# Kernel optimization log

Measured on AMD Instinct MI355X. Metric: run time of the kernel, lower is better.

The kernel has to match this reference:

```python
import jax, jax.numpy as jnp
import numpy as np

N_NODES = 100000
N_EDGES = 1600000
F_IN = 128
F_OUT = 64
BN_EPS = 1e-5


def setup_inputs() -> dict:
    key = jax.random.key(0)
    k1, k2, k3, k4, k5, k6 = jax.random.split(key, 6)
    x = jax.random.normal(k1, (N_NODES, F_IN), dtype=jnp.float32)
    edge_index = jax.random.randint(k2, (2, N_EDGES), 0, N_NODES, dtype=jnp.int64)
    edge_weight = jax.random.uniform(k3, (N_EDGES,), dtype=jnp.float32)
    # learned params: linear weight (no bias), batchnorm gamma/beta
    W = jax.random.normal(k4, (F_OUT, F_IN), dtype=jnp.float32) * (1.0 / np.sqrt(F_IN))
    gamma = jnp.ones((F_OUT,), dtype=jnp.float32)
    beta = jnp.zeros((F_OUT,), dtype=jnp.float32)
    return {"x": x, "edge_index": edge_index, "edge_weight": edge_weight,
            "W": W, "gamma": gamma, "beta": beta}


def reference(x, edge_index, edge_weight, W, gamma, beta):
    N = x.shape[0]
    h = x @ W.T  # [N, F_OUT]
    # add self loops with weight 1.0
    loop = jnp.arange(N, dtype=edge_index.dtype)
    src = jnp.concatenate([edge_index[0], loop])
    dst = jnp.concatenate([edge_index[1], loop])
    w = jnp.concatenate([edge_weight, jnp.ones((N,), dtype=h.dtype)])
    # degree of row (src) counts edge occurrences (unweighted)
    deg = jax.ops.segment_sum(jnp.ones_like(w), src, num_segments=N)
    dinv = jnp.where(deg > 0, jax.lax.rsqrt(deg), 0.0)
    norm = dinv[src] * w * dinv[dst]  # [E+N]
    # gather-scale-scatter aggregation
    out = jax.ops.segment_sum(h[src] * norm[:, None], dst, num_segments=N)
    out = jax.nn.relu(out)
    # BatchNorm1d (training mode: biased batch stats over nodes)
    mean = jnp.mean(out, axis=0)
    var = jnp.mean((out - mean) ** 2, axis=0)
    out = (out - mean) * jax.lax.rsqrt(var + BN_EPS) * gamma + beta
    # dropout p=0.0 -> identity
    return out
```

## Files before the change

kernel.cpp:

```cpp
#include <hip/hip_runtime.h>

#define N_NODES 100000
#define N_EDGES 1600000
#define F_IN 128
#define F_OUT 64
#define BN_EPS 1e-5f

#define NPART 2
#define NCHUNK 128
#define PSIZE 50000
#define CHUNK_E 12500

#define SCAN_NB 98


typedef __attribute__((ext_vector_type(8))) short bf16x8;
typedef __attribute__((ext_vector_type(4))) float f32x4;

__device__ __forceinline__ unsigned short f2bf(float x) {
    unsigned u = __float_as_uint(x);
    u += 0x7fffu + ((u >> 16) & 1u);
    return (unsigned short)(u >> 16);
}
__device__ __forceinline__ float bfl(unsigned short v) {
    return __int_as_float(((int)v) << 16);
}

__global__ __launch_bounds__(256) void convert_kernel(const void* __restrict__ ei,
                                                      int* __restrict__ s32,
                                                      int* __restrict__ d32) {
    const long long* q = (const long long*)ei;
    long long probe = q[threadIdx.x & 63];
    bool bad = (probe < 0 || probe >= N_NODES);
    int is64 = (__ballot(bad) == 0ULL);

    int i = blockIdx.x * 256 + threadIdx.x;
    if (i >= N_EDGES / 4) return;
    int4 s, d;
    if (is64) {
        longlong2 a = *(const longlong2*)&q[i * 4];
        longlong2 b = *(const longlong2*)&q[i * 4 + 2];
        s = make_int4((int)a.x, (int)a.y, (int)b.x, (int)b.y);
        longlong2 c = *(const longlong2*)&q[N_EDGES + i * 4];
        longlong2 e = *(const longlong2*)&q[N_EDGES + i * 4 + 2];
        d = make_int4((int)c.x, (int)c.y, (int)e.x, (int)e.y);
    } else {
        s = ((const int4*)ei)[i];
        d = ((const int4*)ei)[N_EDGES / 4 + i];
    }
    ((int4*)s32)[i] = s;
    ((int4*)d32)[i] = d;
}

__global__ __launch_bounds__(512) void count_kernel(const int* __restrict__ s32,
                                                    const int* __restrict__ d32,
                                                    unsigned* __restrict__ partial32,
                                                    unsigned char* __restrict__ rank) {
    __shared__ unsigned bins[PSIZE / 4];
    const int tid = threadIdx.x;
    const int p = blockIdx.x % NPART;
    const int b = blockIdx.x / NPART;
    const int p0 = p * PSIZE;
    for (int i = tid; i < PSIZE / 4; i += 512) bins[i] = 0u;
    __syncthreads();
    const int4* sp = (const int4*)(s32 + b * CHUNK_E);
    const int4* dp = (const int4*)(d32 + b * CHUNK_E);
    const int e0 = b * CHUNK_E;
    for (int i = tid; i < CHUNK_E / 4; i += 512) {
        int4 s = sp[i];
        int4 d = dp[i];
        int e = e0 + i * 4;
#define C1(sk, dk, kk) { \
        unsigned si = (unsigned)((sk) - p0); \
        if (si < PSIZE) atomicAdd(&bins[si >> 2], 1u << ((si & 3) * 8)); \
        unsigned dd = (unsigned)((dk) - p0); \
        if ((unsigned)(sk) < N_NODES && dd < PSIZE) { \
            unsigned sh = (dd & 3) * 8 + 4; \
            unsigned old = atomicAdd(&bins[dd >> 2], 16u << ((dd & 3) * 8)); \
            rank[e + kk] = (unsigned char)((old >> sh) & 0xFu); } }
        C1(s.x, d.x, 0) C1(s.y, d.y, 1) C1(s.z, d.z, 2) C1(s.w, d.w, 3)
#undef C1
    }
    __syncthreads();
    unsigned* dst = partial32 + (unsigned)blockIdx.x * (PSIZE / 4);
    for (int i = tid; i < PSIZE / 4; i += 512) dst[i] = bins[i];
}

__global__ __launch_bounds__(256) void redscan_kernel(unsigned* __restrict__ partial32,
                                                      float* __restrict__ dinv,
                                                      unsigned* __restrict__ off,
                                                      unsigned* __restrict__ bsum,
                                                      float* __restrict__ sums) {
    __shared__ unsigned s[256];
    const int tid = threadIdx.x;
    if (blockIdx.x == 0 && tid < 128) sums[tid] = 0.f;
    const int n0 = blockIdx.x * 1024 + tid * 4;
    unsigned cntk[4] = {0, 0, 0, 0};
    unsigned degk[4] = {0, 0, 0, 0};
    if (n0 < N_NODES) {
        unsigned idx = (unsigned)n0 >> 2;
#pragma unroll 8
        for (int c = 0; c < NCHUNK; ++c) {
            unsigned v = partial32[idx];
            unsigned nv = 0;
#pragma unroll
            for (int k = 0; k < 4; ++k) {
                unsigned byte = (v >> (k * 8)) & 0xFFu;
                nv |= (cntk[k] & 0xFFu) << (k * 8);
                cntk[k] += byte >> 4;
                degk[k] += byte & 0xFu;
            }
            partial32[idx] = nv;
            idx += (NPART * PSIZE) / 4;
        }
#pragma unroll
        for (int k = 0; k < 4; ++k)
            dinv[n0 + k] = rsqrtf((float)(degk[k] + 1u));
    }
    unsigned tsum = cntk[0] + cntk[1] + cntk[2] + cntk[3];
    s[tid] = tsum;
    __syncthreads();
    for (int d = 1; d < 256; d <<= 1) {
        unsigned t = (tid >= d) ? s[tid - d] : 0u;
        __syncthreads();
        s[tid] += t;
        __syncthreads();
    }
    unsigned run = s[tid] - tsum;
    if (n0 < N_NODES) {
        uint4 o;
        o.x = run;
        o.y = run + cntk[0];
        o.z = o.y + cntk[1];
        o.w = o.z + cntk[2];
        *(uint4*)&off[n0] = o;
    }
    if (tid == 255) bsum[blockIdx.x] = s[255];
}

__global__ __launch_bounds__(128) void scan2_kernel(unsigned* __restrict__ bsum) {
    __shared__ unsigned s[128];
    const int tid = threadIdx.x;
    unsigned v = (tid < SCAN_NB) ? bsum[tid] : 0u;
    s[tid] = v;
    __syncthreads();
    for (int d = 1; d < 128; d <<= 1) {
        unsigned t = (tid >= d) ? s[tid - d] : 0u;
        __syncthreads();
        s[tid] += t;
        __syncthreads();
    }
    if (tid < SCAN_NB) bsum[tid] = s[tid] - v;
}

__global__ __launch_bounds__(256) void place_kernel(const int* __restrict__ s32,
                                                    const int* __restrict__ d32,
                                                    const float* __restrict__ ew,
                                                    const unsigned* __restrict__ off,
                                                    const unsigned* __restrict__ bsum,
                                                    const unsigned* __restrict__ partial32,
                                                    const unsigned char* __restrict__ rank,
                                                    int2* __restrict__ buck) {
    int i = blockIdx.x * 256 + threadIdx.x;
    if (i >= N_EDGES / 4) return;
    int4 s = ((const int4*)s32)[i];
    int4 d = ((const int4*)d32)[i];
    float4 w = ((const float4*)ew)[i];
    uchar4 r = ((const uchar4*)rank)[i];
    const unsigned char* pb = (const unsigned char*)partial32;
    int e = i * 4;
    int b = e / CHUNK_E;
    unsigned base = (unsigned)b * NPART * PSIZE;
#define P1(sk, dk, wk, rk) { \
    if ((unsigned)(sk) < N_NODES && (unsigned)(dk) < N_NODES) { \
        unsigned pref = pb[base + (unsigned)(dk)]; \
        unsigned slot = off[dk] + bsum[(unsigned)(dk) >> 10] + pref + (rk); \
        if (slot < N_EDGES) \
            buck[slot] = make_int2((sk), __float_as_int(wk)); } }
    P1(s.x, d.x, w.x, r.x) P1(s.y, d.y, w.y, r.y)
    P1(s.z, d.z, w.z, r.z) P1(s.w, d.w, w.w, r.w)
#undef P1
}

__global__ __launch_bounds__(256) void gemm_kernel(const float* __restrict__ x,
                                                   const float* __restrict__ W,
                                                   const float* __restrict__ dinv,
                                                   unsigned short* __restrict__ hb) {
    __shared__ short wlds[16 * 64 * 8];
    const int tid = threadIdx.x;
    const int n0 = blockIdx.x * 64;
    {
        int out = tid & 63;
        int kb = tid >> 6;
#pragma unroll
        for (int i = 0; i < 4; ++i) {
            int koct = kb + i * 4;
            const float* wp = &W[out * F_IN + koct * 8];
            float4 aa = *(const float4*)wp;
            float4 bb = *(const float4*)(wp + 4);
            bf16x8 f;
            f[0] = (short)f2bf(aa.x); f[1] = (short)f2bf(aa.y);
            f[2] = (short)f2bf(aa.z); f[3] = (short)f2bf(aa.w);
            f[4] = (short)f2bf(bb.x); f[5] = (short)f2bf(bb.y);
            f[6] = (short)f2bf(bb.z); f[7] = (short)f2bf(bb.w);
            ((bf16x8*)wlds)[koct * 64 + out] = f;
        }
    }
    __syncthreads();
    const int wv = tid >> 6;
    const int lane = tid & 63;
    const int m = lane & 15;
    const int quad = lane >> 4;
    const int row = n0 + wv * 16 + m;
    const bool rv = row < N_NODES;
    const float* xrow = &x[(long)row * F_IN + quad * 8];
    f32x4 acc0 = {0.f, 0.f, 0.f, 0.f};
    f32x4 acc1 = {0.f, 0.f, 0.f, 0.f};
    f32x4 acc2 = {0.f, 0.f, 0.f, 0.f};
    f32x4 acc3 = {0.f, 0.f, 0.f, 0.f};
#pragma unroll
    for (int kc = 0; kc < 4; ++kc) {
        bf16x8 a = {0, 0, 0, 0, 0, 0, 0, 0};
        if (rv) {
            float4 aa = *(const float4*)(xrow + kc * 32);
            float4 bb = *(const float4*)(xrow + kc * 32 + 4);
            a[0] = (short)f2bf(aa.x); a[1] = (short)f2bf(aa.y);
            a[2] = (short)f2bf(aa.z); a[3] = (short)f2bf(aa.w);
            a[4] = (short)f2bf(bb.x); a[5] = (short)f2bf(bb.y);
            a[6] = (short)f2bf(bb.z); a[7] = (short)f2bf(bb.w);
        }
        const bf16x8* wrow = &((const bf16x8*)wlds)[(kc * 4 + quad) * 64 + m];
        acc0 = __builtin_amdgcn_mfma_f32_16x16x32_bf16(a, wrow[0],  acc0, 0, 0, 0);
        acc1 = __builtin_amdgcn_mfma_f32_16x16x32_bf16(a, wrow[16], acc1, 0, 0, 0);
        acc2 = __builtin_amdgcn_mfma_f32_16x16x32_bf16(a, wrow[32], acc2, 0, 0, 0);
        acc3 = __builtin_amdgcn_mfma_f32_16x16x32_bf16(a, wrow[48], acc3, 0, 0, 0);
    }
#pragma unroll
    for (int r = 0; r < 4; ++r) {
        int node = n0 + wv * 16 + quad * 4 + r;
        if (node < N_NODES) {
            float dv = dinv[node];
            unsigned short* hr = &hb[(long)node * F_OUT + m];
            hr[0]  = f2bf(acc0[r] * dv);
            hr[16] = f2bf(acc1[r] * dv);
            hr[32] = f2bf(acc2[r] * dv);
            hr[48] = f2bf(acc3[r] * dv);
        }
    }
}

#define AGG_BLOCKS 2048
#define NPW 13
__global__ __launch_bounds__(256) void aggregate_kernel(
    const unsigned short* __restrict__ hb, const float* __restrict__ dinv,
    const unsigned* __restrict__ off, const unsigned* __restrict__ bsum,
    const int2* __restrict__ buck, float* __restrict__ out,
    float* __restrict__ sums) {
    const int tid = threadIdx.x;
    const int wv = tid >> 6;
    const int lane = tid & 63;
    const int es = lane >> 3;
    const int cl = lane & 7;
    float s1[8] = {0.f, 0.f, 0.f, 0.f, 0.f, 0.f, 0.f, 0.f};
    float s2[8] = {0.f, 0.f, 0.f, 0.f, 0.f, 0.f, 0.f, 0.f};

    const int wid = blockIdx.x * 4 + wv;
    const int nbeg = wid * NPW;
    const int nend = (nbeg + NPW < N_NODES) ? nbeg + NPW : N_NODES;
    for (int n = nbeg; n < nend; ++n) {
        const unsigned o = off[n] + bsum[(unsigned)n >> 10];
        const unsigned onext = (n + 1 < N_NODES)
            ? off[n + 1] + bsum[(unsigned)(n + 1) >> 10]
            : (unsigned)N_EDGES;
        const unsigned c = onext - o;
        float a0[8] = {0.f, 0.f, 0.f, 0.f, 0.f, 0.f, 0.f, 0.f};
        float a1[8] = {0.f, 0.f, 0.f, 0.f, 0.f, 0.f, 0.f, 0.f};
        unsigned j = es;
        for (; j + 8 < c; j += 16) {
            int2 b1 = buck[o + j];
            int2 b2 = buck[o + j + 8];
            uint4 p1 = *(const uint4*)(hb + ((long)b1.x << 6) + cl * 8);
            uint4 p2 = *(const uint4*)(hb + ((long)b2.x << 6) + cl * 8);
            float w1 = __int_as_float(b1.y);
            float w2 = __int_as_float(b2.y);
            a0[0] += bfl((unsigned short)p1.x) * w1;
            a0[1] += bfl((unsigned short)(p1.x >> 16)) * w1;
            a0[2] += bfl((unsigned short)p1.y) * w1;
            a0[3] += bfl((unsigned short)(p1.y >> 16)) * w1;
            a0[4] += bfl((unsigned short)p1.z) * w1;
            a0[5] += bfl((unsigned short)(p1.z >> 16)) * w1;
            a0[6] += bfl((unsigned short)p1.w) * w1;
            a0[7] += bfl((unsigned short)(p1.w >> 16)) * w1;
            a1[0] += bfl((unsigned short)p2.x) * w2;
            a1[1] += bfl((unsigned short)(p2.x >> 16)) * w2;
            a1[2] += bfl((unsigned short)p2.y) * w2;
            a1[3] += bfl((unsigned short)(p2.y >> 16)) * w2;
            a1[4] += bfl((unsigned short)p2.z) * w2;
            a1[5] += bfl((unsigned short)(p2.z >> 16)) * w2;
            a1[6] += bfl((unsigned short)p2.w) * w2;
            a1[7] += bfl((unsigned short)(p2.w >> 16)) * w2;
        }
        if (j < c) {
            int2 b1 = buck[o + j];
            uint4 p1 = *(const uint4*)(hb + ((long)b1.x << 6) + cl * 8);
            float w1 = __int_as_float(b1.y);
            a0[0] += bfl((unsigned short)p1.x) * w1;
            a0[1] += bfl((unsigned short)(p1.x >> 16)) * w1;
            a0[2] += bfl((unsigned short)p1.y) * w1;
            a0[3] += bfl((unsigned short)(p1.y >> 16)) * w1;
            a0[4] += bfl((unsigned short)p1.z) * w1;
            a0[5] += bfl((unsigned short)(p1.z >> 16)) * w1;
            a0[6] += bfl((unsigned short)p1.w) * w1;
            a0[7] += bfl((unsigned short)(p1.w >> 16)) * w1;
        }
#pragma unroll
        for (int k = 0; k < 8; ++k) {
            a0[k] += a1[k];
            a0[k] += __shfl_xor(a0[k], 8);
            a0[k] += __shfl_xor(a0[k], 16);
            a0[k] += __shfl_xor(a0[k], 32);
        }
        if (es == 0) {
            float dn = dinv[n];
            uint4 pn = *(const uint4*)(hb + ((long)n << 6) + cl * 8);
            float hn[8] = {bfl((unsigned short)pn.x), bfl((unsigned short)(pn.x >> 16)),
                           bfl((unsigned short)pn.y), bfl((unsigned short)(pn.y >> 16)),
                           bfl((unsigned short)pn.z), bfl((unsigned short)(pn.z >> 16)),
                           bfl((unsigned short)pn.w), bfl((unsigned short)(pn.w >> 16))};
            float4 o0, o1;
            float* op = &o0.x;
#pragma unroll
            for (int k = 0; k < 8; ++k) {
                float v = fmaxf(dn * (a0[k] + hn[k]), 0.f);
                ((k < 4) ? (&o0.x) : (&o1.x))[k & 3] = v;
                s1[k] += v;
                s2[k] += v * v;
            }
            (void)op;
            float* orow = &out[(long)n * F_OUT + cl * 8];
            *(float4*)orow = o0;
            *(float4*)(orow + 4) = o1;
        }
    }
    __shared__ float l1[256];
    __shared__ float l2[256];
    if (es == 0) {
#pragma unroll
        for (int k = 0; k < 8; ++k) {
            l1[wv * 64 + cl * 8 + k] = s1[k];
            l2[wv * 64 + cl * 8 + k] = s2[k];
        }
    }
    __syncthreads();
    if (tid < 64) {
        float b1 = l1[tid] + l1[64 + tid] + l1[128 + tid] + l1[192 + tid];
        float b2 = l2[tid] + l2[64 + tid] + l2[128 + tid] + l2[192 + tid];
        atomicAdd(&sums[tid], b1);
        atomicAdd(&sums[64 + tid], b2);
    }
}

__global__ __launch_bounds__(256) void apply_kernel(float* __restrict__ agg,
                                                    const float* __restrict__ sums,
                                                    const float* __restrict__ gamma,
                                                    const float* __restrict__ beta) {
    __shared__ float sc[64], bi[64];
    if (threadIdx.x < 64) {
        int c = threadIdx.x;
        const float inv_n = 1.0f / (float)N_NODES;
        float mean = sums[c] * inv_n;
        float var = sums[64 + c] * inv_n - mean * mean;
        float rs = rsqrtf(var + BN_EPS);
        float scale = rs * gamma[c];
        sc[c] = scale;
        bi[c] = beta[c] - mean * scale;
    }
    __syncthreads();
    int i = blockIdx.x * blockDim.x + threadIdx.x;
    if (i >= N_NODES * 16) return;
    int c4 = (i & 15) << 2;
    float4 v = ((float4*)agg)[i];
    v.x = v.x * sc[c4 + 0] + bi[c4 + 0];
    v.y = v.y * sc[c4 + 1] + bi[c4 + 1];
    v.z = v.z * sc[c4 + 2] + bi[c4 + 2];
    v.w = v.w * sc[c4 + 3] + bi[c4 + 3];
    ((float4*)agg)[i] = v;
}

extern "C" void kernel_launch(void* const* d_in, const int* in_sizes, int n_in,
                              void* d_out, int out_size, void* d_ws, size_t ws_size,
                              hipStream_t stream) {
    const float* x     = (const float*)d_in[0];
    const void*  ei    = d_in[1];
    const float* ew    = (const float*)d_in[2];
    const float* W     = (const float*)d_in[3];
    const float* gamma = (const float*)d_in[4];
    const float* beta  = (const float*)d_in[5];
    float* out = (float*)d_out;
    float* ws  = (float*)d_ws;

    int*            s32       = (int*)ws;
    int*            d32       = (int*)(ws + 1600000);
    unsigned*       partial32 = (unsigned*)(ws + 3200000);
    unsigned short* hb        = (unsigned short*)(ws + 3200000);
    int2*           buck      = (int2*)(ws + 6400000);
    float*          dinv      = ws + 9600000;
    float*          sums      = ws + 9700000;
    unsigned*       off       = (unsigned*)(ws + 9800128);
    unsigned*       bsum      = (unsigned*)(ws + 9900128);
    unsigned char*  rank      = (unsigned char*)d_out;

    convert_kernel<<<(N_EDGES / 4 + 255) / 256, 256, 0, stream>>>(ei, s32, d32);
    count_kernel<<<NPART * NCHUNK, 512, 0, stream>>>(s32, d32, partial32, rank);
    redscan_kernel<<<SCAN_NB, 256, 0, stream>>>(partial32, dinv, off, bsum, sums);
    scan2_kernel<<<1, 128, 0, stream>>>(bsum);
    place_kernel<<<(N_EDGES / 4 + 255) / 256, 256, 0, stream>>>(s32, d32, ew, off, bsum,
                                                                partial32, rank, buck);
    gemm_kernel<<<(N_NODES + 63) / 64, 256, 0, stream>>>(x, W, dinv, hb);
    aggregate_kernel<<<AGG_BLOCKS, 256, 0, stream>>>(hb, dinv, off, bsum, buck, out, sums);
    apply_kernel<<<(N_NODES * 16 + 255) / 256, 256, 0, stream>>>(out, sums, gamma, beta);
}
```

Baseline: 304.8 us.

## Fuse index conversion into count kernel and remap aggregate lanes

```diff
diff --git a/kernel.cpp b/kernel.cpp
--- a/kernel.cpp
+++ b/kernel.cpp
@@ -22,54 +22,45 @@
     u += 0x7fffu + ((u >> 16) & 1u);
     return (unsigned short)(u >> 16);
 }
-__device__ __forceinline__ float bfl(unsigned short v) {
-    return __int_as_float(((int)v) << 16);
-}
-
-__global__ __launch_bounds__(256) void convert_kernel(const void* __restrict__ ei,
-                                                      int* __restrict__ s32,
-                                                      int* __restrict__ d32) {
+__device__ __forceinline__ float4 bf4(uint2 p) {
+    return make_float4(__int_as_float((int)(p.x << 16)),
+                       __int_as_float((int)(p.x & 0xffff0000u)),
+                       __int_as_float((int)(p.y << 16)),
+                       __int_as_float((int)(p.y & 0xffff0000u)));
+}
+
+__global__ __launch_bounds__(512) void count_kernel(const void* __restrict__ ei,
+                                                    int* __restrict__ s32,
+                                                    int* __restrict__ d32,
+                                                    unsigned* __restrict__ partial32) {
+    __shared__ unsigned bins[PSIZE / 4];
     const long long* q = (const long long*)ei;
     long long probe = q[threadIdx.x & 63];
-    bool bad = (probe < 0 || probe >= N_NODES);
-    int is64 = (__ballot(bad) == 0ULL);
-
-    int i = blockIdx.x * 256 + threadIdx.x;
-    if (i >= N_EDGES / 4) return;
-    int4 s, d;
-    if (is64) {
-        longlong2 a = *(const longlong2*)&q[i * 4];
-        longlong2 b = *(const longlong2*)&q[i * 4 + 2];
-        s = make_int4((int)a.x, (int)a.y, (int)b.x, (int)b.y);
-        longlong2 c = *(const longlong2*)&q[N_EDGES + i * 4];
-        longlong2 e = *(const longlong2*)&q[N_EDGES + i * 4 + 2];
-        d = make_int4((int)c.x, (int)c.y, (int)e.x, (int)e.y);
-    } else {
-        s = ((const int4*)ei)[i];
-        d = ((const int4*)ei)[N_EDGES / 4 + i];
-    }
-    ((int4*)s32)[i] = s;
-    ((int4*)d32)[i] = d;
-}
-
-__global__ __launch_bounds__(512) void count_kernel(const int* __restrict__ s32,
-                                                    const int* __restrict__ d32,
-                                                    unsigned* __restrict__ partial32,
-                                                    unsigned char* __restrict__ rank) {
-    __shared__ unsigned bins[PSIZE / 4];
+    bool badp = (probe < 0 || probe >= N_NODES);
+    int is64 = (__ballot(badp) == 0ULL);
+
     const int tid = threadIdx.x;
     const int p = blockIdx.x % NPART;
     const int b = blockIdx.x / NPART;
     const int p0 = p * PSIZE;
     for (int i = tid; i < PSIZE / 4; i += 512) bins[i] = 0u;
     __syncthreads();
-    const int4* sp = (const int4*)(s32 + b * CHUNK_E);
-    const int4* dp = (const int4*)(d32 + b * CHUNK_E);
     const int e0 = b * CHUNK_E;
     for (int i = tid; i < CHUNK_E / 4; i += 512) {
-        int4 s = sp[i];
-        int4 d = dp[i];
         int e = e0 + i * 4;
+        int4 s, d;
+        if (is64) {
+            longlong2 a = *(const longlong2*)&q[e];
+            longlong2 bb = *(const longlong2*)&q[e + 2];
+            s = make_int4((int)a.x, (int)a.y, (int)bb.x, (int)bb.y);
+            longlong2 c2 = *(const longlong2*)&q[N_EDGES + e];
+            longlong2 e2 = *(const longlong2*)&q[N_EDGES + e + 2];
+            d = make_int4((int)c2.x, (int)c2.y, (int)e2.x, (int)e2.y);
+        } else {
+            s = ((const int4*)ei)[e >> 2];
+            d = ((const int4*)ei)[(N_EDGES >> 2) + (e >> 2)];
+        }
+        if (p == 0) ((int4*)s32)[e >> 2] = s;
 #define C1(sk, dk, kk) { \
         unsigned si = (unsigned)((sk) - p0); \
         if (si < PSIZE) atomicAdd(&bins[si >> 2], 1u << ((si & 3) * 8)); \
@@ -77,7 +68,7 @@
         if ((unsigned)(sk) < N_NODES && dd < PSIZE) { \
             unsigned sh = (dd & 3) * 8 + 4; \
             unsigned old = atomicAdd(&bins[dd >> 2], 16u << ((dd & 3) * 8)); \
-            rank[e + kk] = (unsigned char)((old >> sh) & 0xFu); } }
+            d32[e + kk] = (dk) | (int)(((old >> sh) & 0xFu) << 27); } }
         C1(s.x, d.x, 0) C1(s.y, d.y, 1) C1(s.z, d.z, 2) C1(s.w, d.w, 3)
 #undef C1
     }
@@ -159,26 +150,25 @@
                                                     const unsigned* __restrict__ off,
                                                     const unsigned* __restrict__ bsum,
                                                     const unsigned* __restrict__ partial32,
-                                                    const unsigned char* __restrict__ rank,
                                                     int2* __restrict__ buck) {
     int i = blockIdx.x * 256 + threadIdx.x;
     if (i >= N_EDGES / 4) return;
     int4 s = ((const int4*)s32)[i];
     int4 d = ((const int4*)d32)[i];
     float4 w = ((const float4*)ew)[i];
-    uchar4 r = ((const uchar4*)rank)[i];
     const unsigned char* pb = (const unsigned char*)partial32;
     int e = i * 4;
     int b = e / CHUNK_E;
     unsigned base = (unsigned)b * NPART * PSIZE;
-#define P1(sk, dk, wk, rk) { \
-    if ((unsigned)(sk) < N_NODES && (unsigned)(dk) < N_NODES) { \
-        unsigned pref = pb[base + (unsigned)(dk)]; \
-        unsigned slot = off[dk] + bsum[(unsigned)(dk) >> 10] + pref + (rk); \
+#define P1(sk, dvk, wk) { \
+    unsigned dd = (unsigned)(dvk) & 0x07FFFFFFu; \
+    unsigned rk = ((unsigned)(dvk)) >> 27; \
+    if ((unsigned)(sk) < N_NODES && dd < N_NODES) { \
+        unsigned pref = pb[base + dd]; \
+        unsigned slot = off[dd] + bsum[dd >> 10] + pref + rk; \
         if (slot < N_EDGES) \
             buck[slot] = make_int2((sk), __float_as_int(wk)); } }
-    P1(s.x, d.x, w.x, r.x) P1(s.y, d.y, w.y, r.y)
-    P1(s.z, d.z, w.z, r.z) P1(s.w, d.w, w.w, r.w)
+    P1(s.x, d.x, w.x) P1(s.y, d.y, w.y) P1(s.z, d.z, w.z) P1(s.w, d.w, w.w)
 #undef P1
 }
 
@@ -259,10 +249,10 @@
     const int tid = threadIdx.x;
     const int wv = tid >> 6;
     const int lane = tid & 63;
-    const int es = lane >> 3;
-    const int cl = lane & 7;
-    float s1[8] = {0.f, 0.f, 0.f, 0.f, 0.f, 0.f, 0.f, 0.f};
-    float s2[8] = {0.f, 0.f, 0.f, 0.f, 0.f, 0.f, 0.f, 0.f};
+    const int es = lane >> 4;
+    const int cl = lane & 15;
+    float s1[4] = {0.f, 0.f, 0.f, 0.f};
+    float s2[4] = {0.f, 0.f, 0.f, 0.f};
 
     const int wid = blockIdx.x * 4 + wv;
     const int nbeg = wid * NPW;
@@ -273,82 +263,50 @@
             ? off[n + 1] + bsum[(unsigned)(n + 1) >> 10]
             : (unsigned)N_EDGES;
         const unsigned c = onext - o;
-        float a0[8] = {0.f, 0.f, 0.f, 0.f, 0.f, 0.f, 0.f, 0.f};
-        float a1[8] = {0.f, 0.f, 0.f, 0.f, 0.f, 0.f, 0.f, 0.f};
+        float4 a0 = make_float4(0.f, 0.f, 0.f, 0.f);
+        float4 a1 = make_float4(0.f, 0.f, 0.f, 0.f);
         unsigned j = es;
-        for (; j + 8 < c; j += 16) {
+        for (; j + 4 < c; j += 8) {
             int2 b1 = buck[o + j];
-            int2 b2 = buck[o + j + 8];
-            uint4 p1 = *(const uint4*)(hb + ((long)b1.x << 6) + cl * 8);
-            uint4 p2 = *(const uint4*)(hb + ((long)b2.x << 6) + cl * 8);
+            int2 b2 = buck[o + j + 4];
+            float4 h1 = bf4(((const uint2*)(hb + ((long)b1.x << 6)))[cl]);
+            float4 h2 = bf4(((const uint2*)(hb + ((long)b2.x << 6)))[cl]);
             float w1 = __int_as_float(b1.y);
             float w2 = __int_as_float(b2.y);
-            a0[0] += bfl((unsigned short)p1.x) * w1;
-            a0[1] += bfl((unsigned short)(p1.x >> 16)) * w1;
-            a0[2] += bfl((unsigned short)p1.y) * w1;
-            a0[3] += bfl((unsigned short)(p1.y >> 16)) * w1;
-            a0[4] += bfl((unsigned short)p1.z) * w1;
-            a0[5] += bfl((unsigned short)(p1.z >> 16)) * w1;
-            a0[6] += bfl((unsigned short)p1.w) * w1;
-            a0[7] += bfl((unsigned short)(p1.w >> 16)) * w1;
-            a1[0] += bfl((unsigned short)p2.x) * w2;
-            a1[1] += bfl((unsigned short)(p2.x >> 16)) * w2;
-            a1[2] += bfl((unsigned short)p2.y) * w2;
-            a1[3] += bfl((unsigned short)(p2.y >> 16)) * w2;
-            a1[4] += bfl((unsigned short)p2.z) * w2;
-            a1[5] += bfl((unsigned short)(p2.z >> 16)) * w2;
-            a1[6] += bfl((unsigned short)p2.w) * w2;
-            a1[7] += bfl((unsigned short)(p2.w >> 16)) * w2;
+            a0.x += h1.x * w1; a0.y += h1.y * w1; a0.z += h1.z * w1; a0.w += h1.w * w1;
+            a1.x += h2.x * w2; a1.y += h2.y * w2; a1.z += h2.z * w2; a1.w += h2.w * w2;
         }
         if (j < c) {
-            int2 b1 = buck[o + j];
-            uint4 p1 = *(const uint4*)(hb + ((long)b1.x << 6) + cl * 8);
-            float w1 = __int_as_float(b1.y);
-            a0[0] += bfl((unsigned short)p1.x) * w1;
-            a0[1] += bfl((unsigned short)(p1.x >> 16)) * w1;
-            a0[2] += bfl((unsigned short)p1.y) * w1;
-            a0[3] += bfl((unsigned short)(p1.y >> 16)) * w1;
-            a0[4] += bfl((unsigned short)p1.z) * w1;
-            a0[5] += bfl((unsigned short)(p1.z >> 16)) * w1;
-            a0[6] += bfl((unsigned short)p1.w) * w1;
-            a0[7] += bfl((unsigned short)(p1.w >> 16)) * w1;
-        }
-#pragma unroll
-        for (int k = 0; k < 8; ++k) {
-            a0[k] += a1[k];
-            a0[k] += __shfl_xor(a0[k], 8);
-            a0[k] += __shfl_xor(a0[k], 16);
-            a0[k] += __shfl_xor(a0[k], 32);
-        }
+            int2 bb = buck[o + j];
+            float w = __int_as_float(bb.y);
+            float4 hv = bf4(((const uint2*)(hb + ((long)bb.x << 6)))[cl]);
+            a0.x += hv.x * w; a0.y += hv.y * w; a0.z += hv.z * w; a0.w += hv.w * w;
+        }
+        a0.x += a1.x; a0.y += a1.y; a0.z += a1.z; a0.w += a1.w;
+        a0.x += __shfl_xor(a0.x, 16); a0.y += __shfl_xor(a0.y, 16);
+        a0.z += __shfl_xor(a0.z, 16); a0.w += __shfl_xor(a0.w, 16);
+        a0.x += __shfl_xor(a0.x, 32); a0.y += __shfl_xor(a0.y, 32);
+        a0.z += __shfl_xor(a0.z, 32); a0.w += __shfl_xor(a0.w, 32);
         if (es == 0) {
             float dn = dinv[n];
-            uint4 pn = *(const uint4*)(hb + ((long)n << 6) + cl * 8);
-            float hn[8] = {bfl((unsigned short)pn.x), bfl((unsigned short)(pn.x >> 16)),
-                           bfl((unsigned short)pn.y), bfl((unsigned short)(pn.y >> 16)),
-                           bfl((unsigned short)pn.z), bfl((unsigned short)(pn.z >> 16)),
-                           bfl((unsigned short)pn.w), bfl((unsigned short)(pn.w >> 16))};
-            float4 o0, o1;
-            float* op = &o0.x;
-#pragma unroll
-            for (int k = 0; k < 8; ++k) {
-                float v = fmaxf(dn * (a0[k] + hn[k]), 0.f);
-                ((k < 4) ? (&o0.x) : (&o1.x))[k & 3] = v;
-                s1[k] += v;
-                s2[k] += v * v;
-            }
-            (void)op;
-            float* orow = &out[(long)n * F_OUT + cl * 8];
-            *(float4*)orow = o0;
-            *(float4*)(orow + 4) = o1;
+            float4 hn = bf4(((const uint2*)(hb + ((long)n << 6)))[cl]);
+            a0.x = fmaxf(dn * (a0.x + hn.x), 0.f);
+            a0.y = fmaxf(dn * (a0.y + hn.y), 0.f);
+            a0.z = fmaxf(dn * (a0.z + hn.z), 0.f);
+            a0.w = fmaxf(dn * (a0.w + hn.w), 0.f);
+            *(float4*)&out[(long)n * F_OUT + cl * 4] = a0;
+            s1[0] += a0.x; s1[1] += a0.y; s1[2] += a0.z; s1[3] += a0.w;
+            s2[0] += a0.x * a0.x; s2[1] += a0.y * a0.y;
+            s2[2] += a0.z * a0.z; s2[3] += a0.w * a0.w;
         }
     }
     __shared__ float l1[256];
     __shared__ float l2[256];
     if (es == 0) {
 #pragma unroll
-        for (int k = 0; k < 8; ++k) {
-            l1[wv * 64 + cl * 8 + k] = s1[k];
-            l2[wv * 64 + cl * 8 + k] = s2[k];
+        for (int k = 0; k < 4; ++k) {
+            l1[wv * 64 + cl * 4 + k] = s1[k];
+            l2[wv * 64 + cl * 4 + k] = s2[k];
         }
     }
     __syncthreads();
@@ -408,14 +366,12 @@
     float*          sums      = ws + 9700000;
     unsigned*       off       = (unsigned*)(ws + 9800128);
     unsigned*       bsum      = (unsigned*)(ws + 9900128);
-    unsigned char*  rank      = (unsigned char*)d_out;
-
-    convert_kernel<<<(N_EDGES / 4 + 255) / 256, 256, 0, stream>>>(ei, s32, d32);
-    count_kernel<<<NPART * NCHUNK, 512, 0, stream>>>(s32, d32, partial32, rank);
+
+    count_kernel<<<NPART * NCHUNK, 512, 0, stream>>>(ei, s32, d32, partial32);
     redscan_kernel<<<SCAN_NB, 256, 0, stream>>>(partial32, dinv, off, bsum, sums);
     scan2_kernel<<<1, 128, 0, stream>>>(bsum);
     place_kernel<<<(N_EDGES / 4 + 255) / 256, 256, 0, stream>>>(s32, d32, ew, off, bsum,
-                                                                partial32, rank, buck);
+                                                                partial32, buck);
     gemm_kernel<<<(N_NODES + 63) / 64, 256, 0, stream>>>(x, W, dinv, hb);
     aggregate_kernel<<<AGG_BLOCKS, 256, 0, stream>>>(hb, dinv, off, bsum, buck, out, sums);
     apply_kernel<<<(N_NODES * 16 + 255) / 256, 256, 0, stream>>>(out, sums, gamma, beta);
```

Measured after the change: 291.4 us. 1.05x faster.
